# Optimization experiments

Hardware: AMD Instinct MI355X
Metric: run time of the kernel (lower is better)

Reference implementation:

```python
import jax, jax.numpy as jnp
import numpy as np

N = 163842          # icosphere level-7 vertex count
IN_FEATS = 64
OUT_FEATS = 64
K = 7               # 1-ring: self + 6 neighbors


def setup_inputs() -> dict:
    key = jax.random.key(0)
    kx, ko, kw, kb = jax.random.split(key, 4)
    x = jax.random.normal(kx, (N, IN_FEATS), dtype=jnp.float32)
    neigh_orders = jax.random.randint(ko, (N * K,), 0, N, dtype=jnp.int64)
    # torch nn.Linear(7*in_feats, out_feats): weight [out, 7*in], bias [out]
    W = jax.random.normal(kw, (OUT_FEATS, K * IN_FEATS), dtype=jnp.float32) * (1.0 / np.sqrt(K * IN_FEATS))
    b = jax.random.normal(kb, (OUT_FEATS,), dtype=jnp.float32) * 0.01
    return {"x": x, "neigh_orders": neigh_orders, "W": W, "b": b}


def reference(x, neigh_orders, W, b):
    n = x.shape[0]
    # gather 7 neighbor feature vectors per node, flatten: [N, 7*in_feats]
    mat = jnp.take(x, neigh_orders, axis=0).reshape(n, K * IN_FEATS)
    # linear layer: [N, 7*in] @ [7*in, out] + [out]
    return mat @ W.T + b
```

## Files before the change

kernel.cpp:

```cpp
#include <hip/hip_runtime.h>
#include <hip/hip_bf16.h>

#define IN_FEATS 64
#define OUT_FEATS 64
#define K_NEIGH 7
#define KDIM (K_NEIGH * IN_FEATS)

typedef __bf16 bf16x8 __attribute__((ext_vector_type(8)));
typedef float  f32x4  __attribute__((ext_vector_type(4)));

__device__ __forceinline__ unsigned short f2bf(float f) {
    union { float f; unsigned int u; } v; v.f = f;
    unsigned int u = v.u;
    unsigned int r = (u + 0x7FFFu + ((u >> 16) & 1u)) >> 16;
    return (unsigned short)r;
}

__device__ __forceinline__ void gld_lds16(const void* gsrc, void* lds) {
    __builtin_amdgcn_global_load_lds(
        (const __attribute__((address_space(1))) void*)gsrc,
        (__attribute__((address_space(3))) void*)lds, 16, 0, 0);
}

__global__ __launch_bounds__(256)
void cast_bf16_all(const float* __restrict__ x, const float* __restrict__ W,
                   __bf16* __restrict__ xb, __bf16* __restrict__ Wb,
                   int nx8, int nw8) {
    int i = blockIdx.x * 256 + threadIdx.x;
    const int stride = gridDim.x * 256;
    const int tot = nx8 + nw8;
    for (; i < tot; i += stride) {
        const float* s; __bf16* d; long j;
        if (i < nx8) { s = x; d = xb; j = i; }
        else         { s = W; d = Wb; j = i - nx8; }
        f32x4 a0 = *(const f32x4*)(s + j * 8);
        f32x4 a1 = *(const f32x4*)(s + j * 8 + 4);
        bf16x8 o;
        o[0] = (__bf16)a0.x; o[1] = (__bf16)a0.y; o[2] = (__bf16)a0.z; o[3] = (__bf16)a0.w;
        o[4] = (__bf16)a1.x; o[5] = (__bf16)a1.y; o[6] = (__bf16)a1.z; o[7] = (__bf16)a1.w;
        *(bf16x8*)(d + j * 8) = o;
    }
}

__global__ __launch_bounds__(256, 3)
void onering_glds(const __bf16* __restrict__ xb,
                  const __bf16* __restrict__ Wb,
                  const int*   __restrict__ neigh,
                  const float* __restrict__ b,
                  float* __restrict__ out,
                  int n)
{
    __shared__ unsigned short lds_w[2][OUT_FEATS * 64];
    __shared__ unsigned short lds_a[2][4][2048];

    const int tid  = threadIdx.x;
    const int w    = tid >> 6;
    const int lane = tid & 63;
    const int lhi  = lane >> 4;
    const int llo  = lane & 15;

    const int rowbase = blockIdx.x * 128 + w * 32;

    int nidx[2][K_NEIGH];
    #pragma unroll
    for (int rt = 0; rt < 2; ++rt) {
        int r  = rowbase + rt * 16 + llo;
        int rr = (r < n) ? r : 0;
        #pragma unroll
        for (int kn = 0; kn < K_NEIGH; ++kn)
            nidx[rt][kn] = neigh[(long)rr * K_NEIGH + kn];
    }

    const int j0  = w * 2, j1 = w * 2 + 1;
    const int wo0 = j0 * 8 + (lane >> 3);
    const int wo1 = j1 * 8 + (lane >> 3);
    const int wc  = (((lane & 7) ^ ((lane >> 3) & 7)) * 8);
    const __bf16* wsrc0 = Wb + (long)wo0 * KDIM + wc;
    const __bf16* wsrc1 = Wb + (long)wo1 * KDIM + wc;

    const int aoff0 = lhi * 8;
    const int aoff1 = lhi * 8 + 32;

    #define ISSUE(kn_, p_) do {                                                 \
        gld_lds16(xb + (((long)nidx[0][kn_]) << 6) + aoff0, &lds_a[p_][w][0]);    \
        gld_lds16(xb + (((long)nidx[0][kn_]) << 6) + aoff1, &lds_a[p_][w][512]);  \
        gld_lds16(xb + (((long)nidx[1][kn_]) << 6) + aoff0, &lds_a[p_][w][1024]); \
        gld_lds16(xb + (((long)nidx[1][kn_]) << 6) + aoff1, &lds_a[p_][w][1536]); \
        gld_lds16(wsrc0 + (kn_) * 64, &lds_w[p_][j0 * 512]);                      \
        gld_lds16(wsrc1 + (kn_) * 64, &lds_w[p_][j1 * 512]);                      \
    } while (0)

    ISSUE(0, 0);
    ISSUE(1, 1);

    f32x4 acc[2][4] = {};

    #pragma unroll
    for (int kn = 0; kn < K_NEIGH; ++kn) {
        const int p = kn & 1;

        if (kn < 6) asm volatile("s_waitcnt vmcnt(6)" ::: "memory");
        else        asm volatile("s_waitcnt vmcnt(0)" ::: "memory");
        __builtin_amdgcn_sched_barrier(0);
        __builtin_amdgcn_s_barrier();
        __builtin_amdgcn_sched_barrier(0);

        bf16x8 bf[2][4];
        #pragma unroll
        for (int h = 0; h < 2; ++h)
            #pragma unroll
            for (int ct = 0; ct < 4; ++ct) {
                const int ocol    = ct * 16 + llo;
                const int klocal  = h * 32 + lhi * 8;
                const int byteoff = (ocol * 128 + klocal * 2) ^ ((ocol & 7) << 4);
                bf[h][ct] = *(const bf16x8*)((const char*)&lds_w[p][0] + byteoff);
            }
        bf16x8 af[2][2];
        #pragma unroll
        for (int rt = 0; rt < 2; ++rt)
            #pragma unroll
            for (int h = 0; h < 2; ++h)
                af[rt][h] = *(const bf16x8*)((const char*)&lds_a[p][w][rt * 1024 + h * 512]
                                             + lane * 16);

        asm volatile("s_waitcnt lgkmcnt(0)" ::: "memory");
        __builtin_amdgcn_sched_barrier(0);
        __builtin_amdgcn_s_barrier();
        __builtin_amdgcn_sched_barrier(0);

        if (kn + 2 <= 6) {
            if (kn == 0) ISSUE(2, 0);
            if (kn == 1) ISSUE(3, 1);
            if (kn == 2) ISSUE(4, 0);
            if (kn == 3) ISSUE(5, 1);
            if (kn == 4) ISSUE(6, 0);
        }

        #pragma unroll
        for (int h = 0; h < 2; ++h)
            #pragma unroll
            for (int ct = 0; ct < 4; ++ct)
                #pragma unroll
                for (int rt = 0; rt < 2; ++rt)
                    acc[rt][ct] = __builtin_amdgcn_mfma_f32_16x16x32_bf16(
                                      af[rt][h], bf[h][ct], acc[rt][ct], 0, 0, 0);
    }
    #undef ISSUE

    #pragma unroll
    for (int ct = 0; ct < 4; ++ct) {
        float bias = b[ct * 16 + llo];
        #pragma unroll
        for (int rt = 0; rt < 2; ++rt)
            #pragma unroll
            for (int j = 0; j < 4; ++j)
                acc[rt][ct][j] += bias;
    }
    #pragma unroll
    for (int rt = 0; rt < 2; ++rt) {
        const int rbase = rowbase + rt * 16 + lhi * 4;
        #pragma unroll
        for (int j = 0; j < 4; ++j) {
            const int r = rbase + j;
            if (r < n) {
                #pragma unroll
                for (int ct = 0; ct < 4; ++ct)
                    out[(long)r * OUT_FEATS + ct * 16 + llo] = acc[rt][ct][j];
            }
        }
    }
}

__global__ __launch_bounds__(512, 4)
void onering_mfma_f32(const float* __restrict__ x,
                      const int*   __restrict__ neigh,
                      const float* __restrict__ W,
                      const float* __restrict__ b,
                      float* __restrict__ out,
                      int n)
{
    __shared__ unsigned short wlds[OUT_FEATS * KDIM];
    const int tid  = threadIdx.x;
    const int wid  = tid >> 6;
    const int lane = tid & 63;
    const int lhi  = lane >> 4;
    const int llo  = lane & 15;

    for (int i = tid; i < (OUT_FEATS * KDIM) / 4; i += 512) {
        f32x4 w4 = *(const f32x4*)(W + i * 4);
        int e   = i * 4;
        int row = e / KDIM;
        ushort4 h;
        h.x = f2bf(w4.x); h.y = f2bf(w4.y); h.z = f2bf(w4.z); h.w = f2bf(w4.w);
        int byteoff = e * 2;
        byteoff ^= ((row & 7) << 4);
        *(ushort4*)((char*)wlds + byteoff) = h;
    }
    __syncthreads();

    const int rowbase = (blockIdx.x * 8 + wid) * 32;
    int nidx[2][K_NEIGH];
    #pragma unroll
    for (int rt = 0; rt < 2; ++rt) {
        int r  = rowbase + rt * 16 + llo;
        int rr = (r < n) ? r : 0;
        #pragma unroll
        for (int kn = 0; kn < K_NEIGH; ++kn)
            nidx[rt][kn] = neigh[(long)rr * K_NEIGH + kn];
    }

    f32x4 acc[2][4] = {};
    #pragma unroll
    for (int kn = 0; kn < K_NEIGH; ++kn) {
        bf16x8 afr[2][2];
        #pragma unroll
        for (int rt = 0; rt < 2; ++rt) {
            const float* xp = x + (long)nidx[rt][kn] * IN_FEATS + lhi * 8;
            #pragma unroll
            for (int h = 0; h < 2; ++h) {
                f32x4 a0 = *(const f32x4*)(xp + h * 32);
                f32x4 a1 = *(const f32x4*)(xp + h * 32 + 4);
                bf16x8 a;
                a[0] = (__bf16)a0.x; a[1] = (__bf16)a0.y;
                a[2] = (__bf16)a0.z; a[3] = (__bf16)a0.w;
                a[4] = (__bf16)a1.x; a[5] = (__bf16)a1.y;
                a[6] = (__bf16)a1.z; a[7] = (__bf16)a1.w;
                afr[rt][h] = a;
            }
        }
        #pragma unroll
        for (int h = 0; h < 2; ++h) {
            const int kk = kn * 2 + h;
            const int klocal = kk * 32 + lhi * 8;
            bf16x8 bfrag[4];
            #pragma unroll
            for (int ct = 0; ct < 4; ++ct) {
                int ocol    = ct * 16 + llo;
                int byteoff = ocol * (KDIM * 2) + klocal * 2;
                byteoff ^= ((ocol & 7) << 4);
                bfrag[ct] = *(const bf16x8*)((const char*)wlds + byteoff);
            }
            #pragma unroll
            for (int ct = 0; ct < 4; ++ct)
                #pragma unroll
                for (int rt = 0; rt < 2; ++rt)
                    acc[rt][ct] = __builtin_amdgcn_mfma_f32_16x16x32_bf16(
                                      afr[rt][h], bfrag[ct], acc[rt][ct], 0, 0, 0);
        }
    }

    #pragma unroll
    for (int ct = 0; ct < 4; ++ct) {
        float bias = b[ct * 16 + llo];
        #pragma unroll
        for (int rt = 0; rt < 2; ++rt)
            #pragma unroll
            for (int j = 0; j < 4; ++j)
                acc[rt][ct][j] += bias;
    }
    #pragma unroll
    for (int rt = 0; rt < 2; ++rt) {
        const int rbase = rowbase + rt * 16 + lhi * 4;
        #pragma unroll
        for (int j = 0; j < 4; ++j) {
            const int r = rbase + j;
            if (r < n) {
                #pragma unroll
                for (int ct = 0; ct < 4; ++ct)
                    out[(long)r * OUT_FEATS + ct * 16 + llo] = acc[rt][ct][j];
            }
        }
    }
}

extern "C" void kernel_launch(void* const* d_in, const int* in_sizes, int n_in,
                              void* d_out, int out_size, void* d_ws, size_t ws_size,
                              hipStream_t stream) {
    const float* x     = (const float*)d_in[0];
    const int*   neigh = (const int*)d_in[1];
    const float* W     = (const float*)d_in[2];
    const float* b     = (const float*)d_in[3];
    float* out = (float*)d_out;

    const int n = in_sizes[0] / IN_FEATS;

    const size_t need = 65536 + (size_t)n * IN_FEATS * sizeof(unsigned short);
    if (ws_size >= need) {
        __bf16* Wb = (__bf16*)d_ws;
        __bf16* xb = (__bf16*)((char*)d_ws + 65536);
        const int nx8 = n * IN_FEATS / 8;
        const int nw8 = OUT_FEATS * KDIM / 8;
        cast_bf16_all<<<dim3(2048), dim3(256), 0, stream>>>(x, W, xb, Wb, nx8, nw8);
        const int nblocks = (n + 127) / 128;
        onering_glds<<<dim3(nblocks), dim3(256), 0, stream>>>(
            xb, Wb, neigh, b, out, n);
    } else {
        const int nblocks = (n + 255) / 256;
        onering_mfma_f32<<<dim3(nblocks), dim3(512), 0, stream>>>(
            x, neigh, W, b, out, n);
    }
}
```

Before: 46.04 us.

## Preload full weight matrix into LDS and use per-wave triple-buffered gathers

The gather kernel now loads the whole bf16 weight matrix (64x448) into swizzled LDS once per block instead of streaming a weight slice for every neighbour step. Each wave gets private triple-buffered LDS for its gathered activation rows, so the block-wide barriers inside the K loop go away. Blocks grow to 512 threads covering 256 rows, with occupancy 1. The cost is a larger LDS footprint of about 155KB per block, a serial weight preload before compute starts, and fewer resident blocks per CU to hide gather latency.

```diff
diff --git a/kernel.cpp b/kernel.cpp
--- a/kernel.cpp
+++ b/kernel.cpp
@@ -42,16 +42,16 @@
     }
 }
 
-__global__ __launch_bounds__(256, 3)
-void onering_glds(const __bf16* __restrict__ xb,
-                  const __bf16* __restrict__ Wb,
-                  const int*   __restrict__ neigh,
-                  const float* __restrict__ b,
-                  float* __restrict__ out,
-                  int n)
+__global__ __launch_bounds__(512, 1)
+void onering_glds2(const __bf16* __restrict__ xb,
+                   const __bf16* __restrict__ Wb,
+                   const int*   __restrict__ neigh,
+                   const float* __restrict__ b,
+                   float* __restrict__ out,
+                   int n)
 {
-    __shared__ unsigned short lds_w[2][OUT_FEATS * 64];
-    __shared__ unsigned short lds_a[2][4][2048];
+    __shared__ unsigned short wlds[OUT_FEATS * KDIM];
+    __shared__ unsigned short lds_a[8][3][2048];
 
     const int tid  = threadIdx.x;
     const int w    = tid >> 6;
@@ -59,7 +59,7 @@
     const int lhi  = lane >> 4;
     const int llo  = lane & 15;
 
-    const int rowbase = blockIdx.x * 128 + w * 32;
+    const int rowbase = blockIdx.x * 256 + w * 32;
 
     int nidx[2][K_NEIGH];
     #pragma unroll
@@ -71,70 +71,68 @@
             nidx[rt][kn] = neigh[(long)rr * K_NEIGH + kn];
     }
 
-    const int j0  = w * 2, j1 = w * 2 + 1;
-    const int wo0 = j0 * 8 + (lane >> 3);
-    const int wo1 = j1 * 8 + (lane >> 3);
-    const int wc  = (((lane & 7) ^ ((lane >> 3) & 7)) * 8);
-    const __bf16* wsrc0 = Wb + (long)wo0 * KDIM + wc;
-    const __bf16* wsrc1 = Wb + (long)wo1 * KDIM + wc;
+    #pragma unroll
+    for (int q = 0; q < 7; ++q) {
+        const int c = tid + q * 512;
+        const int e = c * 8;
+        const int o = e / KDIM;
+        const int k = e % KDIM;
+        bf16x8 v = *(const bf16x8*)(Wb + e);
+        const int dest = (o * (KDIM * 2) + k * 2) ^ ((o & 7) << 4);
+        *(bf16x8*)((char*)wlds + dest) = v;
+    }
+    __syncthreads();
 
     const int aoff0 = lhi * 8;
     const int aoff1 = lhi * 8 + 32;
 
-    #define ISSUE(kn_, p_) do {                                                 \
-        gld_lds16(xb + (((long)nidx[0][kn_]) << 6) + aoff0, &lds_a[p_][w][0]);    \
-        gld_lds16(xb + (((long)nidx[0][kn_]) << 6) + aoff1, &lds_a[p_][w][512]);  \
-        gld_lds16(xb + (((long)nidx[1][kn_]) << 6) + aoff0, &lds_a[p_][w][1024]); \
-        gld_lds16(xb + (((long)nidx[1][kn_]) << 6) + aoff1, &lds_a[p_][w][1536]); \
-        gld_lds16(wsrc0 + (kn_) * 64, &lds_w[p_][j0 * 512]);                      \
-        gld_lds16(wsrc1 + (kn_) * 64, &lds_w[p_][j1 * 512]);                      \
+    #define ISSUE(kn_, p_) do {                                                   \
+        gld_lds16(xb + (((long)nidx[0][kn_]) << 6) + aoff0, &lds_a[w][p_][0]);    \
+        gld_lds16(xb + (((long)nidx[0][kn_]) << 6) + aoff1, &lds_a[w][p_][512]);  \
+        gld_lds16(xb + (((long)nidx[1][kn_]) << 6) + aoff0, &lds_a[w][p_][1024]); \
+        gld_lds16(xb + (((long)nidx[1][kn_]) << 6) + aoff1, &lds_a[w][p_][1536]); \
     } while (0)
 
     ISSUE(0, 0);
     ISSUE(1, 1);
+    ISSUE(2, 2);
 
     f32x4 acc[2][4] = {};
 
     #pragma unroll
     for (int kn = 0; kn < K_NEIGH; ++kn) {
-        const int p = kn & 1;
-
-        if (kn < 6) asm volatile("s_waitcnt vmcnt(6)" ::: "memory");
-        else        asm volatile("s_waitcnt vmcnt(0)" ::: "memory");
+        const int p = kn % 3;
+
+        if (kn <= 4)      asm volatile("s_waitcnt vmcnt(8)" ::: "memory");
+        else if (kn == 5) asm volatile("s_waitcnt vmcnt(4)" ::: "memory");
+        else              asm volatile("s_waitcnt vmcnt(0)" ::: "memory");
         __builtin_amdgcn_sched_barrier(0);
-        __builtin_amdgcn_s_barrier();
-        __builtin_amdgcn_sched_barrier(0);
-
+
+        bf16x8 af[2][2];
+        #pragma unroll
+        for (int rt = 0; rt < 2; ++rt)
+            #pragma unroll
+            for (int h = 0; h < 2; ++h)
+                af[rt][h] = *(const bf16x8*)((const char*)&lds_a[w][p][rt * 1024 + h * 512]
+                                             + lane * 16);
         bf16x8 bf[2][4];
         #pragma unroll
         for (int h = 0; h < 2; ++h)
             #pragma unroll
             for (int ct = 0; ct < 4; ++ct) {
                 const int ocol    = ct * 16 + llo;
-                const int klocal  = h * 32 + lhi * 8;
-                const int byteoff = (ocol * 128 + klocal * 2) ^ ((ocol & 7) << 4);
-                bf[h][ct] = *(const bf16x8*)((const char*)&lds_w[p][0] + byteoff);
-            }
-        bf16x8 af[2][2];
-        #pragma unroll
-        for (int rt = 0; rt < 2; ++rt)
-            #pragma unroll
-            for (int h = 0; h < 2; ++h)
-                af[rt][h] = *(const bf16x8*)((const char*)&lds_a[p][w][rt * 1024 + h * 512]
-                                             + lane * 16);
+                const int klocal  = kn * 64 + h * 32 + lhi * 8;
+                const int byteoff = (ocol * (KDIM * 2) + klocal * 2) ^ ((ocol & 7) << 4);
+                bf[h][ct] = *(const bf16x8*)((const char*)wlds + byteoff);
+            }
 
         asm volatile("s_waitcnt lgkmcnt(0)" ::: "memory");
         __builtin_amdgcn_sched_barrier(0);
-        __builtin_amdgcn_s_barrier();
-        __builtin_amdgcn_sched_barrier(0);
-
-        if (kn + 2 <= 6) {
-            if (kn == 0) ISSUE(2, 0);
-            if (kn == 1) ISSUE(3, 1);
-            if (kn == 2) ISSUE(4, 0);
-            if (kn == 3) ISSUE(5, 1);
-            if (kn == 4) ISSUE(6, 0);
-        }
+
+        if (kn == 0) ISSUE(3, 0);
+        if (kn == 1) ISSUE(4, 1);
+        if (kn == 2) ISSUE(5, 2);
+        if (kn == 3) ISSUE(6, 0);
 
         #pragma unroll
         for (int h = 0; h < 2; ++h)
@@ -291,8 +289,8 @@
         const int nx8 = n * IN_FEATS / 8;
         const int nw8 = OUT_FEATS * KDIM / 8;
         cast_bf16_all<<<dim3(2048), dim3(256), 0, stream>>>(x, W, xb, Wb, nx8, nw8);
-        const int nblocks = (n + 127) / 128;
-        onering_glds<<<dim3(nblocks), dim3(256), 0, stream>>>(
+        const int nblocks = (n + 255) / 256;
+        onering_glds2<<<dim3(nblocks), dim3(512), 0, stream>>>(
             xb, Wb, neigh, b, out, n);
     } else {
         const int nblocks = (n + 255) / 256;
```

New measurement: 48.41 us. +5.2%, slower.
